# Kernel tuning notes

Measured on AMD Instinct MI355X. Metric: run time of the kernel, lower is better.

## Reference

```python
import jax, jax.numpy as jnp
import numpy as np

B, T, C = 2, 2048, 1024
H = 16


def setup_inputs() -> dict:
    key = jax.random.key(0)
    k1, k2, k3 = jax.random.split(key, 3)
    X = jax.random.normal(k1, (B, T, C), dtype=jnp.float32)
    # scale weights like typical inits to keep activations sane
    W_qkv = jax.random.normal(k2, (C, 3 * C), dtype=jnp.float32) / np.sqrt(C)
    W_proj = jax.random.normal(k3, (C, C), dtype=jnp.float32) / np.sqrt(C)
    return {"X": X, "W_qkv": W_qkv, "W_proj": W_proj}


def reference(X, W_qkv, W_proj):
    b, t, c = X.shape
    hd = c // H  # head dim
    qkv = X @ W_qkv  # (B,T,3C)
    q, k, v = jnp.split(qkv, 3, axis=2)
    # (B,H,T,hd)
    q = q.reshape(b, t, H, hd).transpose(0, 2, 1, 3)
    k = k.reshape(b, t, H, hd).transpose(0, 2, 1, 3)
    v = v.reshape(b, t, H, hd).transpose(0, 2, 1, 3)
    att = jnp.einsum("bhqd,bhkd->bhqk", q, k) * (1.0 / np.sqrt(hd))
    causal = jnp.tril(jnp.ones((t, t), dtype=bool))[None, None]
    att = jnp.where(causal, att, -jnp.inf)
    att = jax.nn.softmax(att, axis=-1)
    y = jnp.einsum("bhqk,bhkd->bhqd", att, v)
    y = y.transpose(0, 2, 1, 3).reshape(b, t, c)
    return y @ W_proj
```

## Files before the change

### kernel.cpp

```cpp
#include <hip/hip_runtime.h>
#include <hip/hip_bf16.h>

typedef __attribute__((ext_vector_type(8))) short bf16x8;
typedef __attribute__((ext_vector_type(4))) float f32x4;

#define LOG2E 1.4426950408889634f

__device__ __forceinline__ unsigned short f2b(float f) {
  union { float f; unsigned u; } v; v.f = f;
  unsigned r = v.u + 0x7fffu + ((v.u >> 16) & 1u);
  return (unsigned short)(r >> 16);
}

__device__ __forceinline__ unsigned pack2(float a, float b) {
  __hip_bfloat162 h = __float22bfloat162_rn(make_float2(a, b));
  union { __hip_bfloat162 h; unsigned u; } v;
  v.h = h;
  return v.u;
}

__global__ void cast_x_kernel(const float* __restrict__ X, unsigned short* __restrict__ Xb, int n4) {
  int i = blockIdx.x * blockDim.x + threadIdx.x;
  if (i < n4) {
    float4 v = reinterpret_cast<const float4*>(X)[i];
    ushort4 o = make_ushort4(f2b(v.x), f2b(v.y), f2b(v.z), f2b(v.w));
    reinterpret_cast<ushort4*>(Xb)[i] = o;
  }
}

__global__ void transpose_cast_kernel(const float* __restrict__ W, unsigned short* __restrict__ Wt,
                                      int K, int N) {
  int lane = threadIdx.x & 63;
  int wave = threadIdx.x >> 6;
  int n = blockIdx.x * 64 + lane;
  int k0 = blockIdx.y * 32 + wave * 8;
  bf16x8 v;
#pragma unroll
  for (int j = 0; j < 8; ++j) v[j] = (short)f2b(W[(size_t)(k0 + j) * N + n]);
  *reinterpret_cast<bf16x8*>(&Wt[(size_t)n * K + k0]) = v;
}

__device__ __forceinline__ void stage_tile(const unsigned short* __restrict__ A,
                                           const unsigned short* __restrict__ Bt,
                                           int m0, int n0, int kk, int K,
                                           unsigned short* As, unsigned short* Bs, int tid) {
  int wave = tid >> 6;
  int row = tid >> 2;
  int chunk = tid & 3;
  typedef __attribute__((address_space(3))) unsigned int lds_u32;
  typedef const __attribute__((address_space(1))) unsigned int glb_u32;
  const unsigned short* ga0 = A + (size_t)(m0 + row) * K + kk + chunk * 8;
  const unsigned short* ga1 = A + (size_t)(m0 + 64 + row) * K + kk + chunk * 8;
  const unsigned short* gb0 = Bt + (size_t)(n0 + row) * K + kk + chunk * 8;
  const unsigned short* gb1 = Bt + (size_t)(n0 + 64 + row) * K + kk + chunk * 8;
  __builtin_amdgcn_global_load_lds((glb_u32*)ga0, (lds_u32*)(As + wave * 512), 16, 0, 0);
  __builtin_amdgcn_global_load_lds((glb_u32*)ga1, (lds_u32*)(As + 2048 + wave * 512), 16, 0, 0);
  __builtin_amdgcn_global_load_lds((glb_u32*)gb0, (lds_u32*)(Bs + wave * 512), 16, 0, 0);
  __builtin_amdgcn_global_load_lds((glb_u32*)gb1, (lds_u32*)(Bs + 2048 + wave * 512), 16, 0, 0);
}

template <int MODE>
__launch_bounds__(256, 2)
__global__ void gemm_bt_kernel(const unsigned short* __restrict__ A,
                               const unsigned short* __restrict__ Bt,
                               void* __restrict__ Cout,
                               unsigned short* __restrict__ Vt,
                               int M, int N, int K) {
  __shared__ __align__(16) unsigned short As[2][128 * 32];
  __shared__ __align__(16) unsigned short Bs[2][128 * 32];
  const int tid = threadIdx.x;
  const int lane = tid & 63;
  const int wave = tid >> 6;
  const int wr = wave >> 1, wc = wave & 1;
  const int m0 = blockIdx.y * 128;
  const int n0 = blockIdx.x * 128;
  const int lr = lane & 15;
  const int lk = (lane >> 4) * 8;

  f32x4 zero = {0.f, 0.f, 0.f, 0.f};
  f32x4 acc[4][4];
#pragma unroll
  for (int i = 0; i < 4; ++i)
#pragma unroll
    for (int j = 0; j < 4; ++j) acc[i][j] = zero;

  const int KT = K >> 5;
  stage_tile(A, Bt, m0, n0, 0, K, As[0], Bs[0], tid);
  int buf = 0;
  for (int kt = 0; kt < KT; ++kt) {
    __syncthreads();
    if (kt + 1 < KT) stage_tile(A, Bt, m0, n0, (kt + 1) << 5, K, As[buf ^ 1], Bs[buf ^ 1], tid);
    bf16x8 af[4], bfr[4];
#pragma unroll
    for (int mf = 0; mf < 4; ++mf)
      af[mf] = *reinterpret_cast<const bf16x8*>(&As[buf][(wr * 64 + mf * 16 + lr) * 32 + lk]);
#pragma unroll
    for (int nf = 0; nf < 4; ++nf)
      bfr[nf] = *reinterpret_cast<const bf16x8*>(&Bs[buf][(wc * 64 + nf * 16 + lr) * 32 + lk]);
#pragma unroll
    for (int mf = 0; mf < 4; ++mf)
#pragma unroll
      for (int nf = 0; nf < 4; ++nf)
        acc[mf][nf] = __builtin_amdgcn_mfma_f32_16x16x32_bf16(af[mf], bfr[nf], acc[mf][nf], 0, 0, 0);
    buf ^= 1;
  }

  const int lj = (lane >> 4) * 4;
  if (MODE == 1) {
    float* C = (float*)Cout;
#pragma unroll
    for (int mf = 0; mf < 4; ++mf)
#pragma unroll
      for (int nf = 0; nf < 4; ++nf) {
        int n = n0 + wc * 64 + nf * 16 + lr;
#pragma unroll
        for (int j = 0; j < 4; ++j) {
          int m = m0 + wr * 64 + mf * 16 + lj + j;
          C[(size_t)m * N + n] = acc[mf][nf][j];
        }
      }
  } else {
    unsigned short* QK = (unsigned short*)Cout;
    if (n0 < 2048) {
#pragma unroll
      for (int mf = 0; mf < 4; ++mf)
#pragma unroll
        for (int nf = 0; nf < 4; ++nf) {
          int n = n0 + wc * 64 + nf * 16 + lr;
          float scale = (n < 1024) ? 0.125f : 1.0f;
#pragma unroll
          for (int j = 0; j < 4; ++j) {
            int m = m0 + wr * 64 + mf * 16 + lj + j;
            QK[(size_t)m * 2048 + n] = f2b(acc[mf][nf][j] * scale);
          }
        }
    } else {
#pragma unroll
      for (int mf = 0; mf < 4; ++mf)
#pragma unroll
        for (int nf = 0; nf < 4; ++nf) {
          int n = n0 - 2048 + wc * 64 + nf * 16 + lr;
          int d = n & 63, h = n >> 6;
          int mbase = m0 + wr * 64 + mf * 16 + lj;
          int bb = mbase >> 11, t = mbase & 2047;
          ushort4 v = make_ushort4(f2b(acc[mf][nf][0]), f2b(acc[mf][nf][1]),
                                   f2b(acc[mf][nf][2]), f2b(acc[mf][nf][3]));
          *reinterpret_cast<ushort4*>(&Vt[(((size_t)bb * 16 + h) * 64 + d) * 2048 + t]) = v;
        }
    }
  }
}

#define PFENCE() asm volatile("s_waitcnt lgkmcnt(0)" ::: "memory")

#define KLOAD(TK)                                                                                 \
  {                                                                                               \
    const unsigned short* kp = Kbase + (size_t)((TK) << 6) * 2048;                                \
    _Pragma("unroll")                                                                             \
    for (int nf = 0; nf < 4; ++nf) {                                                              \
      const unsigned short* kq = kp + (size_t)(nf * 16) * 2048;                                   \
      kf[nf][0] = *reinterpret_cast<const bf16x8*>(kq);                                           \
      kf[nf][1] = *reinterpret_cast<const bf16x8*>(kq + 32);                                      \
    }                                                                                             \
  }

#define VLOADX(VF, TK)                                                                            \
  {                                                                                               \
    const unsigned short* vp0 = Vbase + ((TK) << 6);                                              \
    _Pragma("unroll")                                                                             \
    for (int mf = 0; mf < 4; ++mf) {                                                              \
      const unsigned short* vp = vp0 + (size_t)(mf * 16) * 2048;                                  \
      VF[mf][0] = *reinterpret_cast<const bf16x8*>(vp);                                           \
      VF[mf][1] = *reinterpret_cast<const bf16x8*>(vp + 32);                                      \
    }                                                                                             \
  }

#define QKC(ST, QF)                                                                               \
  {                                                                                               \
    __builtin_amdgcn_s_setprio(1);                                                                \
    _Pragma("unroll")                                                                             \
    for (int nf = 0; nf < 4; ++nf) {                                                              \
      ST[nf] = __builtin_amdgcn_mfma_f32_16x16x32_bf16(kf[nf][0], QF[0], zero, 0, 0, 0);          \
      ST[nf] = __builtin_amdgcn_mfma_f32_16x16x32_bf16(kf[nf][1], QF[1], ST[nf], 0, 0, 0);        \
    }                                                                                             \
    __builtin_amdgcn_s_setprio(0);                                                                \
  }

#define MASKST(ST, NFD)                                                                           \
  {                                                                                               \
    _Pragma("unroll")                                                                             \
    for (int nf = 0; nf < 4; ++nf)                                                                \
      _Pragma("unroll")                                                                           \
      for (int j = 0; j < 4; ++j) {                                                               \
        bool kill = (nf > (NFD)) || ((nf == (NFD)) && (4 * lhi + j > lr));                        \
        ST[nf][j] = kill ? -1e30f : ST[nf][j];                                                    \
      }                                                                                           \
  }

#define SMP(ST, MROW, LSUM, ACCO, WOUT)                                                           \
  {                                                                                               \
    float pmax = -1e30f;                                                                          \
    _Pragma("unroll")                                                                             \
    for (int nf = 0; nf < 4; ++nf)                                                                \
      _Pragma("unroll")                                                                           \
      for (int j = 0; j < 4; ++j) pmax = fmaxf(pmax, ST[nf][j]);                                  \
    pmax = fmaxf(pmax, __shfl_xor(pmax, 16));                                                     \
    pmax = fmaxf(pmax, __shfl_xor(pmax, 32));                                                     \
    const float mnew = fmaxf(MROW, pmax);                                                         \
    const float fsc = exp2f((MROW - mnew) * LOG2E);                                               \
    float psum = 0.f;                                                                             \
    _Pragma("unroll")                                                                             \
    for (int nf = 0; nf < 4; ++nf)                                                                \
      _Pragma("unroll")                                                                           \
      for (int h2 = 0; h2 < 2; ++h2) {                                                            \
        float p0 = exp2f((ST[nf][2 * h2] - mnew) * LOG2E);                                        \
        float p1 = exp2f((ST[nf][2 * h2 + 1] - mnew) * LOG2E);                                    \
        psum += p0 + p1;                                                                          \
        WOUT[nf * 2 + h2] = pack2(p0, p1);                                                        \
      }                                                                                           \
    psum += __shfl_xor(psum, 16);                                                                 \
    psum += __shfl_xor(psum, 32);                                                                 \
    LSUM = LSUM * fsc + psum;                                                                     \
    MROW = mnew;                                                                                  \
    _Pragma("unroll")                                                                             \
    for (int mf = 0; mf < 4; ++mf)                                                                \
      _Pragma("unroll")                                                                           \
      for (int j = 0; j < 4; ++j) ACCO[mf][j] *= fsc;                                             \
  }

#define PWRITE(PW, WIN)                                                                           \
  {                                                                                               \
    uint4 w0 = make_uint4(WIN[0], WIN[1], WIN[2], WIN[3]);                                        \
    uint4 w1 = make_uint4(WIN[4], WIN[5], WIN[6], WIN[7]);                                        \
    *reinterpret_cast<uint4*>(&PW[lr][8 * lhi]) = w0;                                             \
    *reinterpret_cast<uint4*>(&PW[lr][8 * lhi + 4]) = w1;                                         \
  }

#define PREAD(PW, PB)                                                                             \
  {                                                                                               \
    _Pragma("unroll")                                                                             \
    for (int kd = 0; kd < 2; ++kd) {                                                              \
      const int nfk = 2 * kd + (lhi >> 1);                                                        \
      const int c = 2 * (nfk & 1) + 4 * (nfk >> 1);                                               \
      const int s0 = 8 * ((2 * lhi) & 3) + c;                                                     \
      const int s1 = 8 * ((2 * lhi + 1) & 3) + c;                                                 \
      union { bf16x8 v; unsigned int u[4]; } pu;                                                  \
      uint2 ra = *reinterpret_cast<const uint2*>(&PW[lr][s0]);                                    \
      uint2 rb = *reinterpret_cast<const uint2*>(&PW[lr][s1]);                                    \
      pu.u[0] = ra.x; pu.u[1] = ra.y; pu.u[2] = rb.x; pu.u[3] = rb.y;                             \
      PB[kd] = pu.v;                                                                              \
    }                                                                                             \
  }

#define PVC(ACCO, VF, PB)                                                                         \
  {                                                                                               \
    __builtin_amdgcn_s_setprio(1);                                                                \
    _Pragma("unroll")                                                                             \
    for (int mf = 0; mf < 4; ++mf) {                                                              \
      ACCO[mf] = __builtin_amdgcn_mfma_f32_16x16x32_bf16(VF[mf][0], PB[0], ACCO[mf], 0, 0, 0);    \
      ACCO[mf] = __builtin_amdgcn_mfma_f32_16x16x32_bf16(VF[mf][1], PB[1], ACCO[mf], 0, 0, 0);    \
    }                                                                                             \
    __builtin_amdgcn_s_setprio(0);                                                                \
  }

#define EPILOG(ACCO, LSUM, Q0)                                                                    \
  {                                                                                               \
    const float inv = 1.0f / LSUM;                                                                \
    unsigned short* Op = O + ((size_t)(b * T + (Q0) + lr)) * 1024 + h * 64 + 4 * lhi;             \
    _Pragma("unroll")                                                                             \
    for (int mf = 0; mf < 4; ++mf) {                                                              \
      uint2 o = make_uint2(pack2(ACCO[mf][0] * inv, ACCO[mf][1] * inv),                           \
                           pack2(ACCO[mf][2] * inv, ACCO[mf][3] * inv));                          \
      *reinterpret_cast<uint2*>(Op + 16 * mf) = o;                                                \
    }                                                                                             \
  }

__launch_bounds__(64)
__global__ void attn_kernel(const unsigned short* __restrict__ QK,
                            const unsigned short* __restrict__ Vt,
                            unsigned short* __restrict__ O) {
  __shared__ unsigned int Pw[2][2][16][36];
  const int T = 2048;
  const int lane = threadIdx.x;
  const int lr = lane & 15;
  const int lhi = lane >> 4;
  const int bh = blockIdx.x & 31;
  const int pid = blockIdx.x >> 5;
  const int b = bh >> 4, h = bh & 15;
  const int qsA = 127 - pid, qsB = pid;
  const int q0A = qsA * 16, q0B = qsB * 16;
  const int ktmaxA = qsA >> 2, ktmaxB = qsB >> 2;
  const int nfdA = qsA & 3, nfdB = qsB & 3;

  const f32x4 zero = {0.f, 0.f, 0.f, 0.f};

  const unsigned short* QpA = QK + ((size_t)(b * T + q0A + lr)) * 2048 + h * 64 + lhi * 8;
  const unsigned short* QpB = QK + ((size_t)(b * T + q0B + lr)) * 2048 + h * 64 + lhi * 8;
  bf16x8 qfA[2] = {*reinterpret_cast<const bf16x8*>(QpA),
                   *reinterpret_cast<const bf16x8*>(QpA + 32)};
  bf16x8 qfB[2] = {*reinterpret_cast<const bf16x8*>(QpB),
                   *reinterpret_cast<const bf16x8*>(QpB + 32)};

  const unsigned short* Kbase = QK + ((size_t)(b * T + lr)) * 2048 + 1024 + h * 64 + lhi * 8;
  const unsigned short* Vbase = Vt + ((size_t)(bh * 64 + lr)) * 2048 + lhi * 8;

  bf16x8 kf[4][2];
  KLOAD(0);

  f32x4 accA[4] = {zero, zero, zero, zero};
  f32x4 accB[4] = {zero, zero, zero, zero};
  float mrowA = -1e30f, lsumA = 0.f, mrowB = -1e30f, lsumB = 0.f;

  for (int kt = 0; kt <= ktmaxA; ++kt) {
    const bool actB = (kt <= ktmaxB);
    const int pp = kt & 1;
    bf16x8 vf[4][2];
    VLOADX(vf, kt);

    f32x4 stA[4], stB[4];
    QKC(stA, qfA);
    if (actB) QKC(stB, qfB);
    {
      int tk = (kt + 1 > ktmaxA) ? ktmaxA : kt + 1;
      KLOAD(tk);
    }
    if (kt == ktmaxA) MASKST(stA, nfdA);
    if (actB && kt == ktmaxB) MASKST(stB, nfdB);

    unsigned WA[8], WB[8];
    SMP(stA, mrowA, lsumA, accA, WA);
    if (actB) SMP(stB, mrowB, lsumB, accB, WB);

    PWRITE(Pw[0][pp], WA);
    if (actB) PWRITE(Pw[1][pp], WB);
    PFENCE();
    bf16x8 pbA[2], pbB[2];
    PREAD(Pw[0][pp], pbA);
    if (actB) PREAD(Pw[1][pp], pbB);

    PVC(accA, vf, pbA);
    if (actB) PVC(accB, vf, pbB);
  }

  EPILOG(accA, lsumA, q0A);
  EPILOG(accB, lsumB, q0B);
}

extern "C" void kernel_launch(void* const* d_in, const int* in_sizes, int n_in,
                              void* d_out, int out_size, void* d_ws, size_t ws_size,
                              hipStream_t stream) {
  const float* X = (const float*)d_in[0];
  const float* Wqkv = (const float*)d_in[1];
  const float* Wproj = (const float*)d_in[2];
  float* out = (float*)d_out;

  char* ws = (char*)d_ws;
  unsigned short* Xb     = (unsigned short*)(ws);
  unsigned short* WqkvT  = (unsigned short*)(ws + 8388608);
  unsigned short* WprojT = (unsigned short*)(ws + 14680064);
  unsigned short* QKb    = (unsigned short*)(ws + 16777216);
  unsigned short* Vt     = (unsigned short*)(ws + 33554432);
  unsigned short* Ob     = (unsigned short*)(ws + 41943040);

  cast_x_kernel<<<4096, 256, 0, stream>>>(X, Xb, 4194304 / 4);
  transpose_cast_kernel<<<dim3(48, 32), 256, 0, stream>>>(Wqkv, WqkvT, 1024, 3072);
  transpose_cast_kernel<<<dim3(16, 32), 256, 0, stream>>>(Wproj, WprojT, 1024, 1024);
  gemm_bt_kernel<0><<<dim3(24, 32), 256, 0, stream>>>(Xb, WqkvT, QKb, Vt, 4096, 3072, 1024);
  attn_kernel<<<2048, 64, 0, stream>>>(QKb, Vt, Ob);
  gemm_bt_kernel<1><<<dim3(8, 32), 256, 0, stream>>>(Ob, WprojT, out, nullptr, 4096, 1024, 1024);
}
```

Measured before the change: 169.5 us.

## Split attention KV range across two waves per block with softmax merge

The attention block grows from one wave to two. Each wave processes half of the key tiles for both query strips (split-K flash attention), and the partial accumulators plus max/sum statistics are merged through shared memory at the end. This shortens the serial per-block loop and doubles the wave count to improve latency hiding. In exchange it adds a __syncthreads, extra LDS traffic and rescaling work, and the two strips are now processed one after the other instead of interleaved, which loses the ILP that came from overlapping them.

```diff
diff --git a/kernel.cpp b/kernel.cpp
--- a/kernel.cpp
+++ b/kernel.cpp
@@ -263,25 +263,39 @@
     __builtin_amdgcn_s_setprio(0);                                                                \
   }
 
-#define EPILOG(ACCO, LSUM, Q0)                                                                    \
-  {                                                                                               \
-    const float inv = 1.0f / LSUM;                                                                \
-    unsigned short* Op = O + ((size_t)(b * T + (Q0) + lr)) * 1024 + h * 64 + 4 * lhi;             \
-    _Pragma("unroll")                                                                             \
-    for (int mf = 0; mf < 4; ++mf) {                                                              \
-      uint2 o = make_uint2(pack2(ACCO[mf][0] * inv, ACCO[mf][1] * inv),                           \
-                           pack2(ACCO[mf][2] * inv, ACCO[mf][3] * inv));                          \
-      *reinterpret_cast<uint2*>(Op + 16 * mf) = o;                                                \
-    }                                                                                             \
-  }
-
-__launch_bounds__(64)
+#define RUN_STRIP(QF, LO, HI, KTMAX, NFD, MROW, LSUM, ACC)                                        \
+  if ((HI) > (LO)) {                                                                              \
+    KLOAD(LO);                                                                                    \
+    for (int kt = (LO); kt < (HI); ++kt) {                                                        \
+      const int pp = kt & 1;                                                                      \
+      bf16x8 vf[4][2];                                                                            \
+      VLOADX(vf, kt);                                                                             \
+      f32x4 st[4];                                                                                \
+      QKC(st, QF);                                                                                \
+      {                                                                                           \
+        int tk = (kt + 1 < (HI)) ? kt + 1 : kt;                                                   \
+        KLOAD(tk);                                                                                \
+      }                                                                                           \
+      if (kt == (KTMAX)) MASKST(st, NFD);                                                         \
+      unsigned W[8];                                                                              \
+      SMP(st, MROW, LSUM, ACC, W);                                                                \
+      PWRITE(Pw[wave][pp], W);                                                                    \
+      PFENCE();                                                                                   \
+      bf16x8 pb[2];                                                                               \
+      PREAD(Pw[wave][pp], pb);                                                                    \
+      PVC(ACC, vf, pb);                                                                           \
+    }                                                                                             \
+  }
+
+__launch_bounds__(128)
 __global__ void attn_kernel(const unsigned short* __restrict__ QK,
                             const unsigned short* __restrict__ Vt,
                             unsigned short* __restrict__ O) {
   __shared__ unsigned int Pw[2][2][16][36];
   const int T = 2048;
-  const int lane = threadIdx.x;
+  const int tid = threadIdx.x;
+  const int wave = tid >> 6;
+  const int lane = tid & 63;
   const int lr = lane & 15;
   const int lhi = lane >> 4;
   const int bh = blockIdx.x & 31;
@@ -289,61 +303,87 @@
   const int b = bh >> 4, h = bh & 15;
   const int qsA = 127 - pid, qsB = pid;
   const int q0A = qsA * 16, q0B = qsB * 16;
-  const int ktmaxA = qsA >> 2, ktmaxB = qsB >> 2;
+  const int nA = (qsA >> 2) + 1, nB = (qsB >> 2) + 1;
+  const int hA = (nA + 1) >> 1, hB = (nB + 1) >> 1;
+  const int loA = wave ? hA : 0, hiA = wave ? nA : hA;
+  const int loB = wave ? hB : 0, hiB = wave ? nB : hB;
+  const int ktmaxA = nA - 1, ktmaxB = nB - 1;
   const int nfdA = qsA & 3, nfdB = qsB & 3;
 
   const f32x4 zero = {0.f, 0.f, 0.f, 0.f};
 
+  const unsigned short* Kbase = QK + ((size_t)(b * T + lr)) * 2048 + 1024 + h * 64 + lhi * 8;
+  const unsigned short* Vbase = Vt + ((size_t)(bh * 64 + lr)) * 2048 + lhi * 8;
+
+  bf16x8 kf[4][2];
+
   const unsigned short* QpA = QK + ((size_t)(b * T + q0A + lr)) * 2048 + h * 64 + lhi * 8;
-  const unsigned short* QpB = QK + ((size_t)(b * T + q0B + lr)) * 2048 + h * 64 + lhi * 8;
   bf16x8 qfA[2] = {*reinterpret_cast<const bf16x8*>(QpA),
                    *reinterpret_cast<const bf16x8*>(QpA + 32)};
+  f32x4 accA[4] = {zero, zero, zero, zero};
+  float mA = -1e30f, lA = 0.f;
+  RUN_STRIP(qfA, loA, hiA, ktmaxA, nfdA, mA, lA, accA);
+
+  const unsigned short* QpB = QK + ((size_t)(b * T + q0B + lr)) * 2048 + h * 64 + lhi * 8;
   bf16x8 qfB[2] = {*reinterpret_cast<const bf16x8*>(QpB),
                    *reinterpret_cast<const bf16x8*>(QpB + 32)};
-
-  const unsigned short* Kbase = QK + ((size_t)(b * T + lr)) * 2048 + 1024 + h * 64 + lhi * 8;
-  const unsigned short* Vbase = Vt + ((size_t)(bh * 64 + lr)) * 2048 + lhi * 8;
-
-  bf16x8 kf[4][2];
-  KLOAD(0);
-
-  f32x4 accA[4] = {zero, zero, zero, zero};
   f32x4 accB[4] = {zero, zero, zero, zero};
-  float mrowA = -1e30f, lsumA = 0.f, mrowB = -1e30f, lsumB = 0.f;
-
-  for (int kt = 0; kt <= ktmaxA; ++kt) {
-    const bool actB = (kt <= ktmaxB);
-    const int pp = kt & 1;
-    bf16x8 vf[4][2];
-    VLOADX(vf, kt);
-
-    f32x4 stA[4], stB[4];
-    QKC(stA, qfA);
-    if (actB) QKC(stB, qfB);
-    {
-      int tk = (kt + 1 > ktmaxA) ? ktmaxA : kt + 1;
-      KLOAD(tk);
+  float mB = -1e30f, lB = 0.f;
+  RUN_STRIP(qfB, loB, hiB, ktmaxB, nfdB, mB, lB, accB);
+
+  float* S = (float*)&Pw[0][0][0][0];
+  {
+    float* dst = S + wave * 1152 + lane * 18;
+    if (wave) {
+#pragma unroll
+      for (int mf = 0; mf < 4; ++mf)
+#pragma unroll
+        for (int j = 0; j < 4; ++j) dst[mf * 4 + j] = accA[mf][j];
+      dst[16] = mA;
+      dst[17] = lA;
+    } else {
+#pragma unroll
+      for (int mf = 0; mf < 4; ++mf)
+#pragma unroll
+        for (int j = 0; j < 4; ++j) dst[mf * 4 + j] = accB[mf][j];
+      dst[16] = mB;
+      dst[17] = lB;
     }
-    if (kt == ktmaxA) MASKST(stA, nfdA);
-    if (actB && kt == ktmaxB) MASKST(stB, nfdB);
-
-    unsigned WA[8], WB[8];
-    SMP(stA, mrowA, lsumA, accA, WA);
-    if (actB) SMP(stB, mrowB, lsumB, accB, WB);
-
-    PWRITE(Pw[0][pp], WA);
-    if (actB) PWRITE(Pw[1][pp], WB);
-    PFENCE();
-    bf16x8 pbA[2], pbB[2];
-    PREAD(Pw[0][pp], pbA);
-    if (actB) PREAD(Pw[1][pp], pbB);
-
-    PVC(accA, vf, pbA);
-    if (actB) PVC(accB, vf, pbB);
-  }
-
-  EPILOG(accA, lsumA, q0A);
-  EPILOG(accB, lsumB, q0B);
+  }
+  __syncthreads();
+  {
+    const float* src = S + (wave ^ 1) * 1152 + lane * 18;
+    const float mO = src[16], lO = src[17];
+    float mS, lS;
+    if (wave) { mS = mB; lS = lB; } else { mS = mA; lS = lA; }
+    const float m = fmaxf(mS, mO);
+    const float a = exp2f((mS - m) * LOG2E);
+    const float bb2 = exp2f((mO - m) * LOG2E);
+    const float inv = 1.0f / (lS * a + lO * bb2);
+    const int q0 = wave ? q0B : q0A;
+    unsigned short* Op = O + ((size_t)(b * T + q0 + lr)) * 1024 + h * 64 + 4 * lhi;
+    if (wave) {
+#pragma unroll
+      for (int mf = 0; mf < 4; ++mf) {
+        float o0 = (accB[mf][0] * a + src[mf * 4 + 0] * bb2) * inv;
+        float o1 = (accB[mf][1] * a + src[mf * 4 + 1] * bb2) * inv;
+        float o2 = (accB[mf][2] * a + src[mf * 4 + 2] * bb2) * inv;
+        float o3 = (accB[mf][3] * a + src[mf * 4 + 3] * bb2) * inv;
+        uint2 o = make_uint2(pack2(o0, o1), pack2(o2, o3));
+        *reinterpret_cast<uint2*>(Op + 16 * mf) = o;
+      }
+    } else {
+#pragma unroll
+      for (int mf = 0; mf < 4; ++mf) {
+        float o0 = (accA[mf][0] * a + src[mf * 4 + 0] * bb2) * inv;
+        float o1 = (accA[mf][1] * a + src[mf * 4 + 1] * bb2) * inv;
+        float o2 = (accA[mf][2] * a + src[mf * 4 + 2] * bb2) * inv;
+        float o3 = (accA[mf][3] * a + src[mf * 4 + 3] * bb2) * inv;
+        uint2 o = make_uint2(pack2(o0, o1), pack2(o2, o3));
+        *reinterpret_cast<uint2*>(Op + 16 * mf) = o;
+      }
+    }
+  }
 }
 
 extern "C" void kernel_launch(void* const* d_in, const int* in_sizes, int n_in,
@@ -366,6 +406,6 @@
   transpose_cast_kernel<<<dim3(48, 32), 256, 0, stream>>>(Wqkv, WqkvT, 1024, 3072);
   transpose_cast_kernel<<<dim3(16, 32), 256, 0, stream>>>(Wproj, WprojT, 1024, 1024);
   gemm_bt_kernel<0><<<dim3(24, 32), 256, 0, stream>>>(Xb, WqkvT, QKb, Vt, 4096, 3072, 1024);
-  attn_kernel<<<2048, 64, 0, stream>>>(QKb, Vt, Ob);
+  attn_kernel<<<2048, 128, 0, stream>>>(QKb, Vt, Ob);
   gemm_bt_kernel<1><<<dim3(8, 32), 256, 0, stream>>>(Ob, WprojT, out, nullptr, 4096, 1024, 1024);
 }
```

Result: slower. 212.9 us (+25.6%).

## Split long causal query row into two key halves with merged softmax

Applied to the files above, without the earlier changes.

The long query tile A is split into a front half and a back half of key tiles, processed as two independent online-softmax streams in the same loop alongside tile B. The partial results are merged at the end by rescaling with the two running maxima. This shortens the serial loop from the full row length to about half, which should expose more independent MFMA work per iteration. In exchange it needs more registers (a second K fragment set, extra V loads and a third accumulator) and more LDS, which may lower occupancy.

```diff
diff --git a/kernel.cpp b/kernel.cpp
--- a/kernel.cpp
+++ b/kernel.cpp
@@ -153,14 +153,14 @@
 
 #define PFENCE() asm volatile("s_waitcnt lgkmcnt(0)" ::: "memory")
 
-#define KLOAD(TK)                                                                                 \
+#define KLOAD(KF, TK)                                                                             \
   {                                                                                               \
     const unsigned short* kp = Kbase + (size_t)((TK) << 6) * 2048;                                \
     _Pragma("unroll")                                                                             \
     for (int nf = 0; nf < 4; ++nf) {                                                              \
       const unsigned short* kq = kp + (size_t)(nf * 16) * 2048;                                   \
-      kf[nf][0] = *reinterpret_cast<const bf16x8*>(kq);                                           \
-      kf[nf][1] = *reinterpret_cast<const bf16x8*>(kq + 32);                                      \
+      KF[nf][0] = *reinterpret_cast<const bf16x8*>(kq);                                           \
+      KF[nf][1] = *reinterpret_cast<const bf16x8*>(kq + 32);                                      \
     }                                                                                             \
   }
 
@@ -175,13 +175,13 @@
     }                                                                                             \
   }
 
-#define QKC(ST, QF)                                                                               \
+#define QKC(ST, QF, KF)                                                                           \
   {                                                                                               \
     __builtin_amdgcn_s_setprio(1);                                                                \
     _Pragma("unroll")                                                                             \
     for (int nf = 0; nf < 4; ++nf) {                                                              \
-      ST[nf] = __builtin_amdgcn_mfma_f32_16x16x32_bf16(kf[nf][0], QF[0], zero, 0, 0, 0);          \
-      ST[nf] = __builtin_amdgcn_mfma_f32_16x16x32_bf16(kf[nf][1], QF[1], ST[nf], 0, 0, 0);        \
+      ST[nf] = __builtin_amdgcn_mfma_f32_16x16x32_bf16(KF[nf][0], QF[0], zero, 0, 0, 0);          \
+      ST[nf] = __builtin_amdgcn_mfma_f32_16x16x32_bf16(KF[nf][1], QF[1], ST[nf], 0, 0, 0);        \
     }                                                                                             \
     __builtin_amdgcn_s_setprio(0);                                                                \
   }
@@ -263,23 +263,11 @@
     __builtin_amdgcn_s_setprio(0);                                                                \
   }
 
-#define EPILOG(ACCO, LSUM, Q0)                                                                    \
-  {                                                                                               \
-    const float inv = 1.0f / LSUM;                                                                \
-    unsigned short* Op = O + ((size_t)(b * T + (Q0) + lr)) * 1024 + h * 64 + 4 * lhi;             \
-    _Pragma("unroll")                                                                             \
-    for (int mf = 0; mf < 4; ++mf) {                                                              \
-      uint2 o = make_uint2(pack2(ACCO[mf][0] * inv, ACCO[mf][1] * inv),                           \
-                           pack2(ACCO[mf][2] * inv, ACCO[mf][3] * inv));                          \
-      *reinterpret_cast<uint2*>(Op + 16 * mf) = o;                                                \
-    }                                                                                             \
-  }
-
 __launch_bounds__(64)
 __global__ void attn_kernel(const unsigned short* __restrict__ QK,
                             const unsigned short* __restrict__ Vt,
                             unsigned short* __restrict__ O) {
-  __shared__ unsigned int Pw[2][2][16][36];
+  __shared__ unsigned int Pw[2][3][16][36];
   const int T = 2048;
   const int lane = threadIdx.x;
   const int lr = lane & 15;
@@ -289,8 +277,12 @@
   const int b = bh >> 4, h = bh & 15;
   const int qsA = 127 - pid, qsB = pid;
   const int q0A = qsA * 16, q0B = qsB * 16;
-  const int ktmaxA = qsA >> 2, ktmaxB = qsB >> 2;
+  const int nA = (qsA >> 2) + 1, nB = (qsB >> 2) + 1;
+  const int hA = (nA + 1) >> 1;
+  const int cAF = hA, cAB = nA - hA, cB = nB;
   const int nfdA = qsA & 3, nfdB = qsB & 3;
+  int maxIter = cAF > cAB ? cAF : cAB;
+  if (cB > maxIter) maxIter = cB;
 
   const f32x4 zero = {0.f, 0.f, 0.f, 0.f};
 
@@ -304,46 +296,104 @@
   const unsigned short* Kbase = QK + ((size_t)(b * T + lr)) * 2048 + 1024 + h * 64 + lhi * 8;
   const unsigned short* Vbase = Vt + ((size_t)(bh * 64 + lr)) * 2048 + lhi * 8;
 
-  bf16x8 kf[4][2];
-  KLOAD(0);
-
-  f32x4 accA[4] = {zero, zero, zero, zero};
-  f32x4 accB[4] = {zero, zero, zero, zero};
-  float mrowA = -1e30f, lsumA = 0.f, mrowB = -1e30f, lsumB = 0.f;
-
-  for (int kt = 0; kt <= ktmaxA; ++kt) {
-    const bool actB = (kt <= ktmaxB);
-    const int pp = kt & 1;
+  bf16x8 kf[4][2], kf2[4][2];
+  KLOAD(kf, 0);
+  KLOAD(kf2, hA);
+
+  f32x4 aAF[4] = {zero, zero, zero, zero};
+  f32x4 aAB[4] = {zero, zero, zero, zero};
+  f32x4 aB[4] = {zero, zero, zero, zero};
+  float mAF = -1e30f, lAF = 0.f;
+  float mAB = -1e30f, lAB = 0.f;
+  float mB = -1e30f, lB = 0.f;
+
+  for (int i = 0; i < maxIter; ++i) {
+    const int pp = i & 1;
+    const bool dAF = i < cAF, dAB = i < cAB, dB = i < cB;
     bf16x8 vf[4][2];
-    VLOADX(vf, kt);
-
-    f32x4 stA[4], stB[4];
-    QKC(stA, qfA);
-    if (actB) QKC(stB, qfB);
+    if (dAF || dB) VLOADX(vf, i);
+
+    if (dAF) {
+      f32x4 st[4];
+      QKC(st, qfA, kf);
+      unsigned W[8];
+      SMP(st, mAF, lAF, aAF, W);
+      PWRITE(Pw[pp][0], W);
+    }
+    if (dB) {
+      f32x4 st[4];
+      QKC(st, qfB, kf);
+      if (i == cB - 1) MASKST(st, nfdB);
+      unsigned W[8];
+      SMP(st, mB, lB, aB, W);
+      PWRITE(Pw[pp][1], W);
+    }
     {
-      int tk = (kt + 1 > ktmaxA) ? ktmaxA : kt + 1;
-      KLOAD(tk);
-    }
-    if (kt == ktmaxA) MASKST(stA, nfdA);
-    if (actB && kt == ktmaxB) MASKST(stB, nfdB);
-
-    unsigned WA[8], WB[8];
-    SMP(stA, mrowA, lsumA, accA, WA);
-    if (actB) SMP(stB, mrowB, lsumB, accB, WB);
-
-    PWRITE(Pw[0][pp], WA);
-    if (actB) PWRITE(Pw[1][pp], WB);
+      int tk = i + 1;
+      if (tk > 31) tk = 31;
+      KLOAD(kf, tk);
+    }
+    if (dAB) {
+      f32x4 st[4];
+      QKC(st, qfA, kf2);
+      if (hA + i == nA - 1) MASKST(st, nfdA);
+      unsigned W[8];
+      SMP(st, mAB, lAB, aAB, W);
+      PWRITE(Pw[pp][2], W);
+    }
+    {
+      int tk = hA + i + 1;
+      if (tk > 31) tk = 31;
+      KLOAD(kf2, tk);
+    }
+    bf16x8 vfb[4][2];
+    if (dAB) VLOADX(vfb, hA + i);
+
     PFENCE();
-    bf16x8 pbA[2], pbB[2];
-    PREAD(Pw[0][pp], pbA);
-    if (actB) PREAD(Pw[1][pp], pbB);
-
-    PVC(accA, vf, pbA);
-    if (actB) PVC(accB, vf, pbB);
-  }
-
-  EPILOG(accA, lsumA, q0A);
-  EPILOG(accB, lsumB, q0B);
+
+    if (dAF) {
+      bf16x8 pb[2];
+      PREAD(Pw[pp][0], pb);
+      PVC(aAF, vf, pb);
+    }
+    if (dB) {
+      bf16x8 pb[2];
+      PREAD(Pw[pp][1], pb);
+      PVC(aB, vf, pb);
+    }
+    if (dAB) {
+      bf16x8 pb[2];
+      PREAD(Pw[pp][2], pb);
+      PVC(aAB, vfb, pb);
+    }
+  }
+
+  {
+    const float m = fmaxf(mAF, mAB);
+    const float xa = exp2f((mAF - m) * LOG2E);
+    const float xb = exp2f((mAB - m) * LOG2E);
+    const float inv = 1.0f / (lAF * xa + lAB * xb);
+    unsigned short* Op = O + ((size_t)(b * T + q0A + lr)) * 1024 + h * 64 + 4 * lhi;
+#pragma unroll
+    for (int mf = 0; mf < 4; ++mf) {
+      float o0 = (aAF[mf][0] * xa + aAB[mf][0] * xb) * inv;
+      float o1 = (aAF[mf][1] * xa + aAB[mf][1] * xb) * inv;
+      float o2 = (aAF[mf][2] * xa + aAB[mf][2] * xb) * inv;
+      float o3 = (aAF[mf][3] * xa + aAB[mf][3] * xb) * inv;
+      uint2 o = make_uint2(pack2(o0, o1), pack2(o2, o3));
+      *reinterpret_cast<uint2*>(Op + 16 * mf) = o;
+    }
+  }
+  {
+    const float inv = 1.0f / lB;
+    unsigned short* Op = O + ((size_t)(b * T + q0B + lr)) * 1024 + h * 64 + 4 * lhi;
+#pragma unroll
+    for (int mf = 0; mf < 4; ++mf) {
+      uint2 o = make_uint2(pack2(aB[mf][0] * inv, aB[mf][1] * inv),
+                           pack2(aB[mf][2] * inv, aB[mf][3] * inv));
+      *reinterpret_cast<uint2*>(Op + 16 * mf) = o;
+    }
+  }
 }
 
 extern "C" void kernel_launch(void* const* d_in, const int* in_sizes, int n_in,
```

Result: slower. 178.8 us (+5.5%).

## Split each attention query tile's KV range into two streams merged at end

Applied to the files above, without the earlier changes.

Before, each block paired a short and a long query tile (A/B) so the work per block was balanced. Now each block handles one 16-row query tile and splits its KV range into a front half and a back half. The two halves are processed as interleaved independent online-softmax streams and merged in the epilogue with rescaling. The grid doubles to 4096 blocks, and the row-sum shuffles move out of the loop to the end. The intent is to shorten the serial dependency chain per block and add parallelism. The cost is uneven block lengths and Q tiles loaded per block rather than shared across a pair.

```diff
diff --git a/kernel.cpp b/kernel.cpp
--- a/kernel.cpp
+++ b/kernel.cpp
@@ -153,14 +153,14 @@
 
 #define PFENCE() asm volatile("s_waitcnt lgkmcnt(0)" ::: "memory")
 
-#define KLOAD(TK)                                                                                 \
+#define KLOAD(KF, TK)                                                                             \
   {                                                                                               \
     const unsigned short* kp = Kbase + (size_t)((TK) << 6) * 2048;                                \
     _Pragma("unroll")                                                                             \
     for (int nf = 0; nf < 4; ++nf) {                                                              \
       const unsigned short* kq = kp + (size_t)(nf * 16) * 2048;                                   \
-      kf[nf][0] = *reinterpret_cast<const bf16x8*>(kq);                                           \
-      kf[nf][1] = *reinterpret_cast<const bf16x8*>(kq + 32);                                      \
+      KF[nf][0] = *reinterpret_cast<const bf16x8*>(kq);                                           \
+      KF[nf][1] = *reinterpret_cast<const bf16x8*>(kq + 32);                                      \
     }                                                                                             \
   }
 
@@ -175,13 +175,13 @@
     }                                                                                             \
   }
 
-#define QKC(ST, QF)                                                                               \
+#define QKC(ST, QF, KF)                                                                           \
   {                                                                                               \
     __builtin_amdgcn_s_setprio(1);                                                                \
     _Pragma("unroll")                                                                             \
     for (int nf = 0; nf < 4; ++nf) {                                                              \
-      ST[nf] = __builtin_amdgcn_mfma_f32_16x16x32_bf16(kf[nf][0], QF[0], zero, 0, 0, 0);          \
-      ST[nf] = __builtin_amdgcn_mfma_f32_16x16x32_bf16(kf[nf][1], QF[1], ST[nf], 0, 0, 0);        \
+      ST[nf] = __builtin_amdgcn_mfma_f32_16x16x32_bf16(KF[nf][0], QF[0], zero, 0, 0, 0);          \
+      ST[nf] = __builtin_amdgcn_mfma_f32_16x16x32_bf16(KF[nf][1], QF[1], ST[nf], 0, 0, 0);        \
     }                                                                                             \
     __builtin_amdgcn_s_setprio(0);                                                                \
   }
@@ -218,9 +218,7 @@
         psum += p0 + p1;                                                                          \
         WOUT[nf * 2 + h2] = pack2(p0, p1);                                                        \
       }                                                                                           \
-    psum += __shfl_xor(psum, 16);                                                                 \
-    psum += __shfl_xor(psum, 32);                                                                 \
-    LSUM = LSUM * fsc + psum;                                                                     \
+    LSUM = LSUM * fsc + psum;                                               \
     MROW = mnew;                                                                                  \
     _Pragma("unroll")                                                                             \
     for (int mf = 0; mf < 4; ++mf)                                                                \
@@ -263,18 +261,6 @@
     __builtin_amdgcn_s_setprio(0);                                                                \
   }
 
-#define EPILOG(ACCO, LSUM, Q0)                                                                    \
-  {                                                                                               \
-    const float inv = 1.0f / LSUM;                                                                \
-    unsigned short* Op = O + ((size_t)(b * T + (Q0) + lr)) * 1024 + h * 64 + 4 * lhi;             \
-    _Pragma("unroll")                                                                             \
-    for (int mf = 0; mf < 4; ++mf) {                                                              \
-      uint2 o = make_uint2(pack2(ACCO[mf][0] * inv, ACCO[mf][1] * inv),                           \
-                           pack2(ACCO[mf][2] * inv, ACCO[mf][3] * inv));                          \
-      *reinterpret_cast<uint2*>(Op + 16 * mf) = o;                                                \
-    }                                                                                             \
-  }
-
 __launch_bounds__(64)
 __global__ void attn_kernel(const unsigned short* __restrict__ QK,
                             const unsigned short* __restrict__ Vt,
@@ -285,65 +271,91 @@
   const int lr = lane & 15;
   const int lhi = lane >> 4;
   const int bh = blockIdx.x & 31;
-  const int pid = blockIdx.x >> 5;
-  const int b = bh >> 4, h = bh & 15;
-  const int qsA = 127 - pid, qsB = pid;
-  const int q0A = qsA * 16, q0B = qsB * 16;
-  const int ktmaxA = qsA >> 2, ktmaxB = qsB >> 2;
-  const int nfdA = qsA & 3, nfdB = qsB & 3;
+  const int qs = 127 - (blockIdx.x >> 5);
+  const int b = bh >> 4, h0 = bh & 15;
+  const int q0 = qs * 16;
+  const int n = (qs >> 2) + 1;
+  const int hsp = (n + 1) >> 1;
+  const int cF = hsp, cB = n - hsp;
+  const int nfd = qs & 3;
 
   const f32x4 zero = {0.f, 0.f, 0.f, 0.f};
 
-  const unsigned short* QpA = QK + ((size_t)(b * T + q0A + lr)) * 2048 + h * 64 + lhi * 8;
-  const unsigned short* QpB = QK + ((size_t)(b * T + q0B + lr)) * 2048 + h * 64 + lhi * 8;
-  bf16x8 qfA[2] = {*reinterpret_cast<const bf16x8*>(QpA),
-                   *reinterpret_cast<const bf16x8*>(QpA + 32)};
-  bf16x8 qfB[2] = {*reinterpret_cast<const bf16x8*>(QpB),
-                   *reinterpret_cast<const bf16x8*>(QpB + 32)};
-
-  const unsigned short* Kbase = QK + ((size_t)(b * T + lr)) * 2048 + 1024 + h * 64 + lhi * 8;
+  const unsigned short* Qp = QK + ((size_t)(b * T + q0 + lr)) * 2048 + h0 * 64 + lhi * 8;
+  bf16x8 qf[2] = {*reinterpret_cast<const bf16x8*>(Qp),
+                  *reinterpret_cast<const bf16x8*>(Qp + 32)};
+
+  const unsigned short* Kbase = QK + ((size_t)(b * T + lr)) * 2048 + 1024 + h0 * 64 + lhi * 8;
   const unsigned short* Vbase = Vt + ((size_t)(bh * 64 + lr)) * 2048 + lhi * 8;
 
-  bf16x8 kf[4][2];
-  KLOAD(0);
-
-  f32x4 accA[4] = {zero, zero, zero, zero};
+  bf16x8 kfF[4][2], kfB[4][2];
+  KLOAD(kfF, 0);
+  if (cB) KLOAD(kfB, hsp);
+
+  f32x4 accF[4] = {zero, zero, zero, zero};
   f32x4 accB[4] = {zero, zero, zero, zero};
-  float mrowA = -1e30f, lsumA = 0.f, mrowB = -1e30f, lsumB = 0.f;
-
-  for (int kt = 0; kt <= ktmaxA; ++kt) {
-    const bool actB = (kt <= ktmaxB);
-    const int pp = kt & 1;
-    bf16x8 vf[4][2];
-    VLOADX(vf, kt);
-
-    f32x4 stA[4], stB[4];
-    QKC(stA, qfA);
-    if (actB) QKC(stB, qfB);
+  float mF = -1e30f, lF = 0.f;
+  float mB = -1e30f, lB = 0.f;
+
+  for (int i = 0; i < cF; ++i) {
+    const int pp = i & 1;
+    const bool dB = i < cB;
+    bf16x8 vfF[4][2], vfB[4][2];
+    VLOADX(vfF, i);
+    if (dB) VLOADX(vfB, hsp + i);
+
+    f32x4 stF[4], stB[4];
+    QKC(stF, qf, kfF);
+    if (dB) QKC(stB, qf, kfB);
     {
-      int tk = (kt + 1 > ktmaxA) ? ktmaxA : kt + 1;
-      KLOAD(tk);
+      int tk = i + 1;
+      if (tk > 31) tk = 31;
+      KLOAD(kfF, tk);
     }
-    if (kt == ktmaxA) MASKST(stA, nfdA);
-    if (actB && kt == ktmaxB) MASKST(stB, nfdB);
-
-    unsigned WA[8], WB[8];
-    SMP(stA, mrowA, lsumA, accA, WA);
-    if (actB) SMP(stB, mrowB, lsumB, accB, WB);
-
-    PWRITE(Pw[0][pp], WA);
-    if (actB) PWRITE(Pw[1][pp], WB);
+    if (dB) {
+      int tk = hsp + i + 1;
+      if (tk > 31) tk = 31;
+      KLOAD(kfB, tk);
+    }
+    if (cB == 0 && i == cF - 1) MASKST(stF, nfd);
+    if (dB && i == cB - 1) MASKST(stB, nfd);
+
+    unsigned WF[8], WB[8];
+    SMP(stF, mF, lF, accF, WF);
+    if (dB) SMP(stB, mB, lB, accB, WB);
+
+    PWRITE(Pw[pp][0], WF);
+    if (dB) PWRITE(Pw[pp][1], WB);
     PFENCE();
-    bf16x8 pbA[2], pbB[2];
-    PREAD(Pw[0][pp], pbA);
-    if (actB) PREAD(Pw[1][pp], pbB);
-
-    PVC(accA, vf, pbA);
-    if (actB) PVC(accB, vf, pbB);
-  }
-
-  EPILOG(accA, lsumA, q0A);
-  EPILOG(accB, lsumB, q0B);
+    bf16x8 pbF[2], pbB[2];
+    PREAD(Pw[pp][0], pbF);
+    if (dB) PREAD(Pw[pp][1], pbB);
+
+    PVC(accF, vfF, pbF);
+    if (dB) PVC(accB, vfB, pbB);
+  }
+
+  lF += __shfl_xor(lF, 16);
+  lF += __shfl_xor(lF, 32);
+  lB += __shfl_xor(lB, 16);
+  lB += __shfl_xor(lB, 32);
+
+  {
+    const float m = fmaxf(mF, mB);
+    const float xa = exp2f((mF - m) * LOG2E);
+    const float xb = exp2f((mB - m) * LOG2E);
+    const float inv = 1.0f / (lF * xa + lB * xb);
+    unsigned short* Op = O + ((size_t)(b * T + q0 + lr)) * 1024 + h0 * 64 + 4 * lhi;
+#pragma unroll
+    for (int mf = 0; mf < 4; ++mf) {
+      float o0 = (accF[mf][0] * xa + accB[mf][0] * xb) * inv;
+      float o1 = (accF[mf][1] * xa + accB[mf][1] * xb) * inv;
+      float o2 = (accF[mf][2] * xa + accB[mf][2] * xb) * inv;
+      float o3 = (accF[mf][3] * xa + accB[mf][3] * xb) * inv;
+      uint2 o = make_uint2(pack2(o0, o1), pack2(o2, o3));
+      *reinterpret_cast<uint2*>(Op + 16 * mf) = o;
+    }
+  }
 }
 
 extern "C" void kernel_launch(void* const* d_in, const int* in_sizes, int n_in,
@@ -366,6 +378,6 @@
   transpose_cast_kernel<<<dim3(48, 32), 256, 0, stream>>>(Wqkv, WqkvT, 1024, 3072);
   transpose_cast_kernel<<<dim3(16, 32), 256, 0, stream>>>(Wproj, WprojT, 1024, 1024);
   gemm_bt_kernel<0><<<dim3(24, 32), 256, 0, stream>>>(Xb, WqkvT, QKb, Vt, 4096, 3072, 1024);
-  attn_kernel<<<2048, 64, 0, stream>>>(QKb, Vt, Ob);
+  attn_kernel<<<4096, 64, 0, stream>>>(QKb, Vt, Ob);
   gemm_bt_kernel<1><<<dim3(8, 32), 256, 0, stream>>>(Ob, WprojT, out, nullptr, 4096, 1024, 1024);
 }
```

After: 201.6 us. +18.9%, slower.
